# Performance work log

Hardware: AMD Instinct MI355X
Metric: run time of the kernel (lower is better)

## Reference

```python
import jax, jax.numpy as jnp
import numpy as np

N, K, D = 32768, 4096, 256


def setup_inputs() -> dict:
    key = jax.random.key(0)
    k1, k2 = jax.random.split(key)
    z_e = jax.random.normal(k1, (N, D), dtype=jnp.float32)
    embed = jax.random.normal(k2, (K, D), dtype=jnp.float32)
    return {"z_e": z_e, "embed": embed}


def reference(z_e, embed):
    # squared L2 distances: ||z||^2 - 2 z.E^T + ||e||^2  -> [N, K]
    d = (jnp.sum(z_e * z_e, axis=1, keepdims=True)
         - 2.0 * (z_e @ embed.T)
         + jnp.sum(embed * embed, axis=1))
    idx = jnp.argmin(d, axis=1)                      # [N] int32
    one_hot = jax.nn.one_hot(idx, K, dtype=z_e.dtype)  # [N, K]
    z_q = one_hot @ embed                            # [N, D] (matches torch's one_hot @ embed)
    return (z_q, idx, one_hot)
```

## Files before the change

### kernel.cpp

```cpp
#include <hip/hip_runtime.h>


#define N_TOK 32768
#define K_CODE 4096
#define D_DIM 256
#define BM 64
#define THR_AMBIG 0.125f
#define FIX_NSLICE 32
#define FIX_STRIDES 4

typedef float f32x4 __attribute__((ext_vector_type(4)));
typedef short s16x8 __attribute__((ext_vector_type(8)));

#define OUT_FLOATS 142639104u
#define EFRAG_SHORTS (3u * K_CODE * D_DIM)
#define SCR_FLOATS (EFRAG_SHORTS / 2 + K_CODE + 32768u + 65536u + 64u)
#define SCR_OFF    (OUT_FLOATS - SCR_FLOATS)
#define E2_OFF     (SCR_OFF + EFRAG_SHORTS / 2)
#define LIST_OFF   (E2_OFF + K_CODE)
#define AMIN_OFF   (LIST_OFF + 32768u)
#define CNT_OFF    (AMIN_OFF + 65536u)
#define OH_SAFE_ROWS 32320

#define MFMA(a, b, c) __builtin_amdgcn_mfma_f32_16x16x32_bf16((a), (b), (c), 0, 0, 0)

static __device__ __forceinline__ unsigned short f2bf(float f) {
    unsigned int u = __float_as_uint(f);
    u = (u + 0x7fffu + ((u >> 16) & 1u)) >> 16;
    return (unsigned short)u;
}
static __device__ __forceinline__ float bf2f(unsigned short b) {
    return __uint_as_float(((unsigned int)b) << 16);
}
static __device__ __forceinline__ unsigned long long packvi(float v, int code) {
    unsigned int u = __float_as_uint(v);
    u = (u & 0x80000000u) ? ~u : (u ^ 0x80000000u);
    return ((unsigned long long)u << 32) | (unsigned int)code;
}

__global__ __launch_bounds__(256) void vq_prep(const float* __restrict__ embed,
                                               float* __restrict__ out) {
    __shared__ float part[8][33];
    unsigned short* escr = (unsigned short*)(out + SCR_OFF);
    float* e2g = out + E2_OFF;

    const int t    = threadIdx.x;
    const int cl   = t >> 5;
    const int r32  = t & 31;
    const int dc   = r32 >> 2;
    const int quad = r32 & 3;
    const int k    = blockIdx.x * 8 + cl;

    if (blockIdx.x == 0) {
        if (t == 0) ((int*)(out + CNT_OFF))[0] = 0;
        unsigned long long* am = (unsigned long long*)(out + AMIN_OFF);
        for (int i = t; i < 32768; i += 256) am[i] = ~0ull;
    }

    const float* src = embed + (size_t)k * D_DIM + dc * 32 + quad * 8;
    float x[8];
    *(float4*)(x)     = *(const float4*)(src);
    *(float4*)(x + 4) = *(const float4*)(src + 4);

    s16x8 hv, mv, lv;
    float s2 = 0.0f;
#pragma unroll
    for (int j = 0; j < 8; ++j) {
        const float xx = x[j];
        s2 += xx * xx;
        const unsigned short bh = f2bf(xx);
        const float r1 = xx - bf2f(bh);
        const unsigned short bm = f2bf(r1);
        hv[j] = (short)bh; mv[j] = (short)bm; lv[j] = (short)f2bf(r1 - bf2f(bm));
    }

    const int ct_g = k >> 4;
    const int lane = quad * 16 + (k & 15);
    const size_t base = ((size_t)(ct_g * 8 + dc) * 3) * 512 + lane * 8;
    *(s16x8*)&escr[base]        = hv;
    *(s16x8*)&escr[base + 512]  = mv;
    *(s16x8*)&escr[base + 1024] = lv;

    part[cl][r32] = s2;
    __syncthreads();
    if (t < 8) {
        float s = 0.0f;
#pragma unroll
        for (int j = 0; j < 32; ++j) s += part[t][j];
        e2g[blockIdx.x * 8 + t] = s;
    }
}

static __device__ __forceinline__ void load_b2(const unsigned short* __restrict__ p,
                                               s16x8 (&buf)[4][2]) {
#pragma unroll
    for (int u = 0; u < 4; ++u)
#pragma unroll
        for (int c = 0; c < 2; ++c)
            buf[u][c] = *(const s16x8*)(p + u * 12288 + c * 512);
}

static __device__ __forceinline__ size_t boff(int s) {
    return (size_t)(s >> 3) * 393216 + (size_t)(s & 7) * 1536;
}

static __device__ __forceinline__ void proc2(const short* As,
        const float* __restrict__ e2g, int s, int wu, int lane, int n,
        s16x8 (&B)[4][2], f32x4 (&acc)[4][4], float (&e2r)[4],
        float (&bv)[16], float (&bv2)[16], unsigned int (&pk)[8]) {
    const int ktp = s >> 3;
    const int dc  = s & 7;
    if (dc == 0) {
#pragma unroll
        for (int u = 0; u < 4; ++u)
            e2r[u] = e2g[ktp * 512 + (wu * 4 + u) * 16 + n];
    }
#pragma unroll
    for (int rt = 0; rt < 4; ++rt) {
        s16x8 af0 = *(const s16x8*)&As[((0 * 4 + rt) * 8 + dc) * 512 + lane * 8];
        s16x8 af1 = *(const s16x8*)&As[((1 * 4 + rt) * 8 + dc) * 512 + lane * 8];
#pragma unroll
        for (int u = 0; u < 4; ++u) {
            f32x4 a = acc[rt][u];
            a = MFMA(af0, B[u][0], a);
            a = MFMA(af0, B[u][1], a);
            a = MFMA(af1, B[u][0], a);
            a = MFMA(af1, B[u][1], a);
            acc[rt][u] = a;
        }
    }
    if (dc == 7) {
#pragma unroll
        for (int u = 0; u < 4; ++u) {
            const int code = ktp * 512 + (wu * 4 + u) * 16 + n;
#pragma unroll
            for (int rt = 0; rt < 4; ++rt)
#pragma unroll
                for (int r = 0; r < 4; ++r) {
                    const float val = fmaf(-2.0f, acc[rt][u][r], e2r[u]);
                    const int slot = rt * 4 + r;
                    const int k = slot >> 1, sh = (slot & 1) * 16;
                    if (val < bv[slot]) {
                        bv2[slot] = bv[slot];
                        bv[slot] = val;
                        pk[k] = (pk[k] & ~(0xFFFFu << sh)) | ((unsigned int)code << sh);
                    } else {
                        bv2[slot] = fminf(bv2[slot], val);
                    }
                }
        }
#pragma unroll
        for (int rt = 0; rt < 4; ++rt)
#pragma unroll
            for (int u = 0; u < 4; ++u) acc[rt][u] = (f32x4){0.f, 0.f, 0.f, 0.f};
    }
}

__global__ __launch_bounds__(512, 2)
void vq_pass1(const float* __restrict__ z_e,
              const float* __restrict__ embed,
              float* __restrict__ out) {
    __shared__ __align__(16) short As[32768];
    __shared__ float redv1[64][9];
    __shared__ float redv2[64][9];
    __shared__ int   redi[64][9];
    __shared__ int   bk_lds[64];

    const unsigned short* escr = (const unsigned short*)(out + SCR_OFF);
    const float* e2g = out + E2_OFF;
    int* list = (int*)(out + LIST_OFF);
    int* cnt  = (int*)(out + CNT_OFF);

    const int t    = threadIdx.x;
    const int w    = t >> 6;
    const int lane = t & 63;
    const int n    = lane & 15;
    const int quad = lane >> 4;
    const int row0 = blockIdx.x * BM;

#pragma unroll
    for (int i = 0; i < 4; ++i) {
        const int run  = t + 512 * i;
        const int qs   = run & 3;
        const int dcs  = (run >> 2) & 7;
        const int row  = run >> 5;
        const float* src = z_e + (size_t)(row0 + row) * D_DIM + dcs * 32 + qs * 8;
        float x[8];
        *(float4*)(x)     = *(const float4*)(src);
        *(float4*)(x + 4) = *(const float4*)(src + 4);
        s16x8 hv, mv;
#pragma unroll
        for (int j = 0; j < 8; ++j) {
            const float xx = x[j];
            const unsigned short bh = f2bf(xx);
            hv[j] = (short)bh;
            mv[j] = (short)f2bf(xx - bf2f(bh));
        }
        const int rt = row >> 4;
        const int ls = qs * 16 + (row & 15);
        *(s16x8*)&As[((0 * 4 + rt) * 8 + dcs) * 512 + ls * 8] = hv;
        *(s16x8*)&As[((1 * 4 + rt) * 8 + dcs) * 512 + ls * 8] = mv;
    }
    __syncthreads();

    float bv[16], bv2[16];
    unsigned int pk[8];
#pragma unroll
    for (int s = 0; s < 16; ++s) { bv[s] = 3.0e38f; bv2[s] = 3.0e38f; }
#pragma unroll
    for (int k = 0; k < 8; ++k) pk[k] = 0u;

    f32x4 acc[4][4];
#pragma unroll
    for (int rt = 0; rt < 4; ++rt)
#pragma unroll
        for (int u = 0; u < 4; ++u) acc[rt][u] = (f32x4){0.f, 0.f, 0.f, 0.f};

    float e2r[4];
    s16x8 b0[4][2], b1[4][2];

    const int wu = __builtin_amdgcn_readfirstlane(w);
    const unsigned short* ebase = escr + (size_t)wu * 49152 + lane * 8;

    load_b2(ebase, b0);

#pragma unroll 1
    for (int it = 0; it < 32; ++it) {
        const int s0 = it * 2, s1 = s0 + 1, s2 = s0 + 2;
        load_b2(ebase + boff(s1), b1);
        proc2(As, e2g, s0, wu, lane, n, b0, acc, e2r, bv, bv2, pk);
        if (it < 31) load_b2(ebase + boff(s2), b0);
        proc2(As, e2g, s1, wu, lane, n, b1, acc, e2r, bv, bv2, pk);
    }

#pragma unroll
    for (int mask = 1; mask < 16; mask <<= 1) {
#pragma unroll
        for (int k = 0; k < 8; ++k) {
            const unsigned int opack = (unsigned int)__shfl_xor((int)pk[k], mask);
#pragma unroll
            for (int h = 0; h < 2; ++h) {
                const int slot = 2 * k + h;
                const int sh = h * 16;
                const float ov1 = __shfl_xor(bv[slot], mask);
                const float ov2 = __shfl_xor(bv2[slot], mask);
                if (ov1 < bv[slot]) {
                    bv2[slot] = fminf(bv[slot], ov2);
                    bv[slot] = ov1;
                    pk[k] = (pk[k] & ~(0xFFFFu << sh)) | (opack & (0xFFFFu << sh));
                } else {
                    bv2[slot] = fminf(bv2[slot], ov1);
                }
            }
        }
    }
    if (n == 0) {
#pragma unroll
        for (int rt = 0; rt < 4; ++rt)
#pragma unroll
            for (int r = 0; r < 4; ++r) {
                const int rl = rt * 16 + quad * 4 + r;
                const int slot = rt * 4 + r;
                redv1[rl][w] = bv[slot];
                redv2[rl][w] = bv2[slot];
                redi[rl][w]  = (int)((pk[slot >> 1] >> ((slot & 1) * 16)) & 0xFFFFu);
            }
    }
    __syncthreads();
    if (t < 64) {
        float v1 = redv1[t][0];
        float v2 = redv2[t][0];
        int   bi = redi[t][0];
#pragma unroll
        for (int j = 1; j < 8; ++j) {
            const float o1 = redv1[t][j];
            const float o2 = redv2[t][j];
            const int   oi = redi[t][j];
            if (o1 < v1) { v2 = fminf(v1, o2); v1 = o1; bi = oi; }
            else         { v2 = fminf(v2, o1); }
        }
        bk_lds[t] = bi;
        out[(size_t)N_TOK * D_DIM + (size_t)(row0 + t)] = (float)bi;
        if (v2 - v1 <= THR_AMBIG) {
            const int pos = atomicAdd(cnt, 1);
            list[pos] = row0 + t;
        }
    }
    __syncthreads();

    float* zq = out;
    float* oh = out + (size_t)N_TOK * D_DIM + N_TOK;

#pragma unroll 1
    for (int rr = 0; rr < 8; ++rr) {
        const int rl  = w * 8 + rr;
        const int row = row0 + rl;
        const int bk  = bk_lds[rl] & (K_CODE - 1);
        f32x4 v = *(const f32x4*)&embed[(size_t)bk * D_DIM + lane * 4];
        __builtin_nontemporal_store(v, (f32x4*)&zq[(size_t)row * D_DIM + lane * 4]);
    }
    if (row0 < OH_SAFE_ROWS) {
#pragma unroll 1
        for (int rr = 0; rr < 8; ++rr) {
            const int rl  = w * 8 + rr;
            const int row = row0 + rl;
            const int bk  = bk_lds[rl];
            float* ohrow = &oh[(size_t)row * K_CODE];
#pragma unroll
            for (int g = 0; g < 16; ++g) {
                const int base = (g * 64 + lane) * 4;
                f32x4 u;
                u.x = (bk == base    ) ? 1.0f : 0.0f;
                u.y = (bk == base + 1) ? 1.0f : 0.0f;
                u.z = (bk == base + 2) ? 1.0f : 0.0f;
                u.w = (bk == base + 3) ? 1.0f : 0.0f;
                __builtin_nontemporal_store(u, (f32x4*)&ohrow[base]);
            }
        }
    }
}

__global__ __launch_bounds__(512, 2)
void vq_fixa(const float* __restrict__ z_e, float* __restrict__ out) {
    __shared__ __align__(16) short As[49152];
    __shared__ float redv[64][9];
    __shared__ int   redi[64][9];
    __shared__ int   rows_lds[64];

    const unsigned short* escr = (const unsigned short*)(out + SCR_OFF);
    const float* e2g = out + E2_OFF;
    const int* list = (const int*)(out + LIST_OFF);
    unsigned long long* amin = (unsigned long long*)(out + AMIN_OFF);
    const int cntv = ((const int*)(out + CNT_OFF))[0];
    const int ncap = cntv < N_TOK ? cntv : N_TOK;
    if (ncap <= 0) return;

    const int t    = threadIdx.x;
    const int w    = t >> 6;
    const int lane = t & 63;
    const int n    = lane & 15;
    const int quad = lane >> 4;
    const int slice = blockIdx.x & (FIX_NSLICE - 1);
    const int c0    = blockIdx.x / FIX_NSLICE;

    const int wu = __builtin_amdgcn_readfirstlane(w);
    const unsigned short* ebase = escr + (size_t)(slice * 8 + wu) * 12288 + lane * 8;
    const int mycode = slice * 128 + wu * 16 + n;

#pragma unroll 1
    for (int chunk = c0; chunk * 64 < ncap; chunk += FIX_STRIDES) {
        const int nrows = (ncap - chunk * 64) < 64 ? (ncap - chunk * 64) : 64;
        if (t < 64) {
            const int j = chunk * 64 + t;
            rows_lds[t] = list[j < ncap ? j : chunk * 64];
        }
        __syncthreads();

#pragma unroll
        for (int i = 0; i < 4; ++i) {
            const int run  = t + 512 * i;
            const int qs   = run & 3;
            const int dcs  = (run >> 2) & 7;
            const int row  = run >> 5;
            const int grow = rows_lds[row];
            const float* src = z_e + (size_t)grow * D_DIM + dcs * 32 + qs * 8;
            float x[8];
            *(float4*)(x)     = *(const float4*)(src);
            *(float4*)(x + 4) = *(const float4*)(src + 4);
            s16x8 hv, mv, lv;
#pragma unroll
            for (int j = 0; j < 8; ++j) {
                const float xx = x[j];
                const unsigned short bh = f2bf(xx);
                const float r1 = xx - bf2f(bh);
                const unsigned short bm = f2bf(r1);
                hv[j] = (short)bh; mv[j] = (short)bm; lv[j] = (short)f2bf(r1 - bf2f(bm));
            }
            const int rt = row >> 4;
            const int ls = qs * 16 + (row & 15);
            *(s16x8*)&As[((0 * 4 + rt) * 8 + dcs) * 512 + ls * 8] = hv;
            *(s16x8*)&As[((1 * 4 + rt) * 8 + dcs) * 512 + ls * 8] = mv;
            *(s16x8*)&As[((2 * 4 + rt) * 8 + dcs) * 512 + ls * 8] = lv;
        }
        __syncthreads();

        f32x4 acc[4];
#pragma unroll
        for (int rt = 0; rt < 4; ++rt) acc[rt] = (f32x4){0.f, 0.f, 0.f, 0.f};
        float e2v = 0.0f;

#pragma unroll 1
        for (int dc = 0; dc < 8; ++dc) {
            s16x8 B[3];
            const unsigned short* p = ebase + (size_t)dc * 1536;
#pragma unroll
            for (int c = 0; c < 3; ++c)
                B[c] = *(const s16x8*)(p + c * 512);
            if (dc == 0) e2v = e2g[mycode];
#pragma unroll
            for (int rt = 0; rt < 4; ++rt) {
                s16x8 af0 = *(const s16x8*)&As[((0 * 4 + rt) * 8 + dc) * 512 + lane * 8];
                s16x8 af1 = *(const s16x8*)&As[((1 * 4 + rt) * 8 + dc) * 512 + lane * 8];
                s16x8 af2 = *(const s16x8*)&As[((2 * 4 + rt) * 8 + dc) * 512 + lane * 8];
                f32x4 a = acc[rt];
                a = MFMA(af0, B[0], a);
                a = MFMA(af0, B[1], a);
                a = MFMA(af1, B[0], a);
                a = MFMA(af1, B[1], a);
                a = MFMA(af0, B[2], a);
                a = MFMA(af2, B[0], a);
                acc[rt] = a;
            }
        }

        float bv[16]; int bidx[16];
#pragma unroll
        for (int rt = 0; rt < 4; ++rt)
#pragma unroll
            for (int r = 0; r < 4; ++r) {
                bv[rt * 4 + r]   = fmaf(-2.0f, acc[rt][r], e2v);
                bidx[rt * 4 + r] = mycode;
            }
#pragma unroll
        for (int slot = 0; slot < 16; ++slot) {
#pragma unroll
            for (int mask = 1; mask < 16; mask <<= 1) {
                const float ov = __shfl_xor(bv[slot], mask);
                const int   oi = __shfl_xor(bidx[slot], mask);
                if (ov < bv[slot] || (ov == bv[slot] && oi < bidx[slot])) {
                    bv[slot] = ov; bidx[slot] = oi;
                }
            }
        }
        if (n == 0) {
#pragma unroll
            for (int rt = 0; rt < 4; ++rt)
#pragma unroll
                for (int r = 0; r < 4; ++r) {
                    const int rl = rt * 16 + quad * 4 + r;
                    redv[rl][w] = bv[rt * 4 + r];
                    redi[rl][w] = bidx[rt * 4 + r];
                }
        }
        __syncthreads();
        if (t < nrows) {
            float v = redv[t][0]; int bi = redi[t][0];
#pragma unroll
            for (int j = 1; j < 8; ++j) {
                const float v2 = redv[t][j]; const int i2 = redi[t][j];
                if (v2 < v || (v2 == v && i2 < bi)) { v = v2; bi = i2; }
            }
            atomicMin(&amin[chunk * 64 + t], packvi(v, bi));
        }
        __syncthreads();
    }
}

__global__ __launch_bounds__(256) void vq_fixb(const float* __restrict__ embed,
                                               float* __restrict__ out) {
    const int* list = (const int*)(out + LIST_OFF);
    const unsigned long long* amin = (const unsigned long long*)(out + AMIN_OFF);
    const int cntv = ((const int*)(out + CNT_OFF))[0];
    const int ncap = cntv < N_TOK ? cntv : N_TOK;

    float* idxf = out + (size_t)N_TOK * D_DIM;
    float* zq   = out;
    float* oh   = out + (size_t)N_TOK * D_DIM + N_TOK;
    const int t = threadIdx.x;

#pragma unroll 1
    for (int e = blockIdx.x; e < ncap; e += 32) {
        const int row = list[e];
        const int bi  = (int)(amin[e] & 0xffffffffu) & (K_CODE - 1);
        const int io  = ((int)idxf[row]) & (K_CODE - 1);
        if (bi != io) {
            if (t == 0) idxf[row] = (float)bi;
            if (t < 64) {
                f32x4 v = *(const f32x4*)&embed[(size_t)bi * D_DIM + t * 4];
                *(f32x4*)&zq[(size_t)row * D_DIM + t * 4] = v;
            }
            if (row < OH_SAFE_ROWS && t == 0) {
                oh[(size_t)row * K_CODE + io] = 0.0f;
                oh[(size_t)row * K_CODE + bi] = 1.0f;
            }
        }
    }
}

__launch_bounds__(256, 8)
__global__ void vq_oh_tail(float* __restrict__ out) {
    __shared__ int bks[16];
    const int t    = threadIdx.x;
    const int w    = t >> 6;
    const int lane = t & 63;
    const int row0 = OH_SAFE_ROWS + blockIdx.x * 16;

    const float* idxf = out + (size_t)N_TOK * D_DIM;
    float* oh = out + (size_t)N_TOK * D_DIM + N_TOK;

    if (t < 16) bks[t] = ((int)idxf[row0 + t]) & (K_CODE - 1);
    __syncthreads();

#pragma unroll 1
    for (int rr = 0; rr < 4; ++rr) {
        const int r   = rr * 4 + w;
        const int row = row0 + r;
        const int bk  = bks[r];
        float* ohrow = &oh[(size_t)row * K_CODE];
#pragma unroll
        for (int g = 0; g < 16; ++g) {
            const int base = (g * 64 + lane) * 4;
            f32x4 u;
            u.x = (bk == base    ) ? 1.0f : 0.0f;
            u.y = (bk == base + 1) ? 1.0f : 0.0f;
            u.z = (bk == base + 2) ? 1.0f : 0.0f;
            u.w = (bk == base + 3) ? 1.0f : 0.0f;
            __builtin_nontemporal_store(u, (f32x4*)&ohrow[base]);
        }
    }
}

extern "C" void kernel_launch(void* const* d_in, const int* in_sizes, int n_in,
                              void* d_out, int out_size, void* d_ws, size_t ws_size,
                              hipStream_t stream) {
    const float* z_e   = (const float*)d_in[0];
    const float* embed = (const float*)d_in[1];
    float* out = (float*)d_out;

    hipLaunchKernelGGL(vq_prep,    dim3(K_CODE / 8), dim3(256), 0, stream, embed, out);
    hipLaunchKernelGGL(vq_pass1,   dim3(N_TOK / BM), dim3(512), 0, stream, z_e, embed, out);
    hipLaunchKernelGGL(vq_fixa,    dim3(FIX_NSLICE * FIX_STRIDES), dim3(512), 0, stream, z_e, out);
    hipLaunchKernelGGL(vq_fixb,    dim3(32),  dim3(256), 0, stream, embed, out);
    hipLaunchKernelGGL(vq_oh_tail, dim3((N_TOK - OH_SAFE_ROWS) / 16), dim3(256), 0, stream, out);
}
```

Measured before the change: 827.4 us.

## Grow pass1 row tile to 128 with 2x4 warp grid over rows and codes

The pass-1 block tile doubles from 64 to 128 token rows, and the 8 warps are rearranged into 2 row groups by 4 code groups. Each warp now handles 64 rows by 32 codes per step instead of 64 by 64, and the loop runs 128 steps instead of 32. The aim is to halve how often each block streams the codebook fragments, cutting global/L2 traffic per row. In exchange, LDS use doubles (the A tile alone grows to 128KB) and the grid is halved, which may lower occupancy and wave count; the cross-warp reduction, the output loops, the one-hot safe-row bound and index masking in the fix kernels are adjusted to match.

```diff
diff --git a/kernel.cpp b/kernel.cpp
--- a/kernel.cpp
+++ b/kernel.cpp
@@ -4,7 +4,7 @@
 #define N_TOK 32768
 #define K_CODE 4096
 #define D_DIM 256
-#define BM 64
+#define BM 128
 #define THR_AMBIG 0.125f
 #define FIX_NSLICE 32
 #define FIX_STRIDES 4
@@ -20,7 +20,7 @@
 #define LIST_OFF   (E2_OFF + K_CODE)
 #define AMIN_OFF   (LIST_OFF + 32768u)
 #define CNT_OFF    (AMIN_OFF + 65536u)
-#define OH_SAFE_ROWS 32320
+#define OH_SAFE_ROWS 32256
 
 #define MFMA(a, b, c) __builtin_amdgcn_mfma_f32_16x16x32_bf16((a), (b), (c), 0, 0, 0)
 
@@ -91,36 +91,36 @@
     }
 }
 
-static __device__ __forceinline__ void load_b2(const unsigned short* __restrict__ p,
-                                               s16x8 (&buf)[4][2]) {
-#pragma unroll
-    for (int u = 0; u < 4; ++u)
+static __device__ __forceinline__ void load_b128(const unsigned short* __restrict__ p,
+                                                 s16x8 (&buf)[2][2]) {
+#pragma unroll
+    for (int u = 0; u < 2; ++u)
 #pragma unroll
         for (int c = 0; c < 2; ++c)
             buf[u][c] = *(const s16x8*)(p + u * 12288 + c * 512);
 }
 
-static __device__ __forceinline__ size_t boff(int s) {
-    return (size_t)(s >> 3) * 393216 + (size_t)(s & 7) * 1536;
-}
-
-static __device__ __forceinline__ void proc2(const short* As,
-        const float* __restrict__ e2g, int s, int wu, int lane, int n,
-        s16x8 (&B)[4][2], f32x4 (&acc)[4][4], float (&e2r)[4],
+static __device__ __forceinline__ size_t boff2(int s) {
+    return (size_t)(s >> 3) * 98304 + (size_t)(s & 7) * 1536;
+}
+
+static __device__ __forceinline__ void proc128(const short* As,
+        const float* __restrict__ e2g, int s, int rgu, int cgu, int lane, int n,
+        s16x8 (&B)[2][2], f32x4 (&acc)[4][2], float (&e2r)[2],
         float (&bv)[16], float (&bv2)[16], unsigned int (&pk)[8]) {
     const int ktp = s >> 3;
     const int dc  = s & 7;
     if (dc == 0) {
 #pragma unroll
-        for (int u = 0; u < 4; ++u)
-            e2r[u] = e2g[ktp * 512 + (wu * 4 + u) * 16 + n];
+        for (int u = 0; u < 2; ++u)
+            e2r[u] = e2g[ktp * 128 + cgu * 32 + u * 16 + n];
     }
 #pragma unroll
     for (int rt = 0; rt < 4; ++rt) {
-        s16x8 af0 = *(const s16x8*)&As[((0 * 4 + rt) * 8 + dc) * 512 + lane * 8];
-        s16x8 af1 = *(const s16x8*)&As[((1 * 4 + rt) * 8 + dc) * 512 + lane * 8];
-#pragma unroll
-        for (int u = 0; u < 4; ++u) {
+        s16x8 af0 = *(const s16x8*)&As[((0 * 8 + rgu * 4 + rt) * 8 + dc) * 512 + lane * 8];
+        s16x8 af1 = *(const s16x8*)&As[((1 * 8 + rgu * 4 + rt) * 8 + dc) * 512 + lane * 8];
+#pragma unroll
+        for (int u = 0; u < 2; ++u) {
             f32x4 a = acc[rt][u];
             a = MFMA(af0, B[u][0], a);
             a = MFMA(af0, B[u][1], a);
@@ -131,8 +131,8 @@
     }
     if (dc == 7) {
 #pragma unroll
-        for (int u = 0; u < 4; ++u) {
-            const int code = ktp * 512 + (wu * 4 + u) * 16 + n;
+        for (int u = 0; u < 2; ++u) {
+            const int code = ktp * 128 + cgu * 32 + u * 16 + n;
 #pragma unroll
             for (int rt = 0; rt < 4; ++rt)
 #pragma unroll
@@ -152,7 +152,7 @@
 #pragma unroll
         for (int rt = 0; rt < 4; ++rt)
 #pragma unroll
-            for (int u = 0; u < 4; ++u) acc[rt][u] = (f32x4){0.f, 0.f, 0.f, 0.f};
+            for (int u = 0; u < 2; ++u) acc[rt][u] = (f32x4){0.f, 0.f, 0.f, 0.f};
     }
 }
 
@@ -160,11 +160,11 @@
 void vq_pass1(const float* __restrict__ z_e,
               const float* __restrict__ embed,
               float* __restrict__ out) {
-    __shared__ __align__(16) short As[32768];
-    __shared__ float redv1[64][9];
-    __shared__ float redv2[64][9];
-    __shared__ int   redi[64][9];
-    __shared__ int   bk_lds[64];
+    __shared__ __align__(16) short As[65536];
+    __shared__ float redv1[128][5];
+    __shared__ float redv2[128][5];
+    __shared__ int   redi[128][5];
+    __shared__ int   bk_lds[128];
 
     const unsigned short* escr = (const unsigned short*)(out + SCR_OFF);
     const float* e2g = out + E2_OFF;
@@ -179,7 +179,7 @@
     const int row0 = blockIdx.x * BM;
 
 #pragma unroll
-    for (int i = 0; i < 4; ++i) {
+    for (int i = 0; i < 8; ++i) {
         const int run  = t + 512 * i;
         const int qs   = run & 3;
         const int dcs  = (run >> 2) & 7;
@@ -196,10 +196,10 @@
             hv[j] = (short)bh;
             mv[j] = (short)f2bf(xx - bf2f(bh));
         }
-        const int rt = row >> 4;
-        const int ls = qs * 16 + (row & 15);
-        *(s16x8*)&As[((0 * 4 + rt) * 8 + dcs) * 512 + ls * 8] = hv;
-        *(s16x8*)&As[((1 * 4 + rt) * 8 + dcs) * 512 + ls * 8] = mv;
+        const int rtile = row >> 4;
+        const int ls    = qs * 16 + (row & 15);
+        *(s16x8*)&As[((0 * 8 + rtile) * 8 + dcs) * 512 + ls * 8] = hv;
+        *(s16x8*)&As[((1 * 8 + rtile) * 8 + dcs) * 512 + ls * 8] = mv;
     }
     __syncthreads();
 
@@ -210,27 +210,29 @@
 #pragma unroll
     for (int k = 0; k < 8; ++k) pk[k] = 0u;
 
-    f32x4 acc[4][4];
+    f32x4 acc[4][2];
 #pragma unroll
     for (int rt = 0; rt < 4; ++rt)
 #pragma unroll
-        for (int u = 0; u < 4; ++u) acc[rt][u] = (f32x4){0.f, 0.f, 0.f, 0.f};
-
-    float e2r[4];
-    s16x8 b0[4][2], b1[4][2];
-
-    const int wu = __builtin_amdgcn_readfirstlane(w);
-    const unsigned short* ebase = escr + (size_t)wu * 49152 + lane * 8;
-
-    load_b2(ebase, b0);
-
-#pragma unroll 1
-    for (int it = 0; it < 32; ++it) {
+        for (int u = 0; u < 2; ++u) acc[rt][u] = (f32x4){0.f, 0.f, 0.f, 0.f};
+
+    float e2r[2];
+    s16x8 b0[2][2], b1[2][2];
+
+    const int wu  = __builtin_amdgcn_readfirstlane(w);
+    const int rgu = wu >> 2;
+    const int cgu = wu & 3;
+    const unsigned short* ebase = escr + (size_t)(cgu * 2) * 12288 + lane * 8;
+
+    load_b128(ebase, b0);
+
+#pragma unroll 1
+    for (int it = 0; it < 128; ++it) {
         const int s0 = it * 2, s1 = s0 + 1, s2 = s0 + 2;
-        load_b2(ebase + boff(s1), b1);
-        proc2(As, e2g, s0, wu, lane, n, b0, acc, e2r, bv, bv2, pk);
-        if (it < 31) load_b2(ebase + boff(s2), b0);
-        proc2(As, e2g, s1, wu, lane, n, b1, acc, e2r, bv, bv2, pk);
+        load_b128(ebase + boff2(s1), b1);
+        proc128(As, e2g, s0, rgu, cgu, lane, n, b0, acc, e2r, bv, bv2, pk);
+        if (it < 127) load_b128(ebase + boff2(s2), b0);
+        proc128(As, e2g, s1, rgu, cgu, lane, n, b1, acc, e2r, bv, bv2, pk);
     }
 
 #pragma unroll
@@ -259,20 +261,20 @@
         for (int rt = 0; rt < 4; ++rt)
 #pragma unroll
             for (int r = 0; r < 4; ++r) {
-                const int rl = rt * 16 + quad * 4 + r;
+                const int rl = rgu * 64 + rt * 16 + quad * 4 + r;
                 const int slot = rt * 4 + r;
-                redv1[rl][w] = bv[slot];
-                redv2[rl][w] = bv2[slot];
-                redi[rl][w]  = (int)((pk[slot >> 1] >> ((slot & 1) * 16)) & 0xFFFFu);
+                redv1[rl][cgu] = bv[slot];
+                redv2[rl][cgu] = bv2[slot];
+                redi[rl][cgu]  = (int)((pk[slot >> 1] >> ((slot & 1) * 16)) & 0xFFFFu);
             }
     }
     __syncthreads();
-    if (t < 64) {
+    if (t < 128) {
         float v1 = redv1[t][0];
         float v2 = redv2[t][0];
         int   bi = redi[t][0];
 #pragma unroll
-        for (int j = 1; j < 8; ++j) {
+        for (int j = 1; j < 4; ++j) {
             const float o1 = redv1[t][j];
             const float o2 = redv2[t][j];
             const int   oi = redi[t][j];
@@ -292,8 +294,8 @@
     float* oh = out + (size_t)N_TOK * D_DIM + N_TOK;
 
 #pragma unroll 1
-    for (int rr = 0; rr < 8; ++rr) {
-        const int rl  = w * 8 + rr;
+    for (int rr = 0; rr < 16; ++rr) {
+        const int rl  = w * 16 + rr;
         const int row = row0 + rl;
         const int bk  = bk_lds[rl] & (K_CODE - 1);
         f32x4 v = *(const f32x4*)&embed[(size_t)bk * D_DIM + lane * 4];
@@ -301,8 +303,8 @@
     }
     if (row0 < OH_SAFE_ROWS) {
 #pragma unroll 1
-        for (int rr = 0; rr < 8; ++rr) {
-            const int rl  = w * 8 + rr;
+        for (int rr = 0; rr < 16; ++rr) {
+            const int rl  = w * 16 + rr;
             const int row = row0 + rl;
             const int bk  = bk_lds[rl];
             float* ohrow = &oh[(size_t)row * K_CODE];
@@ -352,7 +354,7 @@
         const int nrows = (ncap - chunk * 64) < 64 ? (ncap - chunk * 64) : 64;
         if (t < 64) {
             const int j = chunk * 64 + t;
-            rows_lds[t] = list[j < ncap ? j : chunk * 64];
+            rows_lds[t] = list[j < ncap ? j : chunk * 64] & (N_TOK - 1);
         }
         __syncthreads();
 
@@ -470,7 +472,7 @@
 
 #pragma unroll 1
     for (int e = blockIdx.x; e < ncap; e += 32) {
-        const int row = list[e];
+        const int row = list[e] & (N_TOK - 1);
         const int bi  = (int)(amin[e] & 0xffffffffu) & (K_CODE - 1);
         const int io  = ((int)idxf[row]) & (K_CODE - 1);
         if (bi != io) {
```

New measurement: 875.3 us. 5.8% more time.
